# Optimization experiments

Measured on AMD Instinct MI355X. Metric: run time of the kernel, lower is better.

Reference implementation:

```python
import jax, jax.numpy as jnp
import numpy as np

# Per-chromosome bin counts: round(len/100000) for hg38 chromosome lengths (from __init__)
CHROM_BINS = [2490, 2422, 1983, 1902, 1815, 1708, 1593, 1451, 1384, 1338, 1351,
              1333, 1144, 1070, 1020, 903, 833, 804, 586, 644, 467, 508]
LOC = np.concatenate([[0], np.cumsum(CHROM_BINS)])  # 23 boundaries, LOC[-1] == 28749
TOTAL_BINS = int(LOC[-1])
COMP = 50          # compression_size
N_HEADS = 22
INPUT_DIM = N_HEADS * COMP * 2  # 2200
H1, H2, OUT = 1000, 50, 13
BATCH = 2048


def setup_inputs() -> dict:
    key = jax.random.key(0)
    ks = jax.random.split(key, 12)
    s = 0.02
    return {
        "input_tensor": jax.random.normal(ks[0], (BATCH, 2, TOTAL_BINS), jnp.float32),
        # all 22 head weight matrices concatenated along the input dim: (COMP, TOTAL_BINS)
        "head_w": jax.random.normal(ks[1], (COMP, TOTAL_BINS), jnp.float32) * s,
        "head_b": jax.random.normal(ks[2], (N_HEADS, COMP), jnp.float32) * s,
        "conc_w": jax.random.normal(ks[3], (INPUT_DIM, INPUT_DIM), jnp.float32) * s,
        "conc_b": jax.random.normal(ks[4], (INPUT_DIM,), jnp.float32) * s,
        "w1": jax.random.normal(ks[5], (H1, INPUT_DIM), jnp.float32) * s,
        "b1": jax.random.normal(ks[6], (H1,), jnp.float32) * s,
        "w2": jax.random.normal(ks[7], (H2, H1), jnp.float32) * s,
        "b2": jax.random.normal(ks[8], (H2,), jnp.float32) * s,
        "w3": jax.random.normal(ks[9], (OUT, H2), jnp.float32) * s,
        "b3": jax.random.normal(ks[10], (OUT,), jnp.float32) * s,
    }


def reference(input_tensor, head_w, head_b, conc_w, conc_b, w1, b1, w2, b2, w3, b3):
    # 22 per-chromosome heads, each applied to both channels; output order per
    # chromosome i is [head_i(ch0), head_i(ch1)], matching the torch loop.
    pieces = []
    for i in range(N_HEADS):
        a, b = int(LOC[i]), int(LOC[i + 1])
        seg = input_tensor[:, :, a:b]                       # (B, 2, L_i)
        h = jnp.einsum('bcl,ol->bco', seg, head_w[:, a:b]) + head_b[i]  # (B, 2, COMP)
        pieces.append(h.reshape(h.shape[0], -1))            # (B, 2*COMP)
    combined = jnp.concatenate(pieces, axis=1)              # (B, 2200)
    z = combined @ conc_w.T + conc_b                        # conc Linear
    # seq: Linear -> Dropout(eval=id) -> LeakyReLU -> Linear -> Dropout -> LeakyReLU -> Dropout -> Linear
    h1 = jax.nn.leaky_relu(z @ w1.T + b1, 0.01)
    h2 = jax.nn.leaky_relu(h1 @ w2.T + b2, 0.01)
    return h2 @ w3.T + b3                                   # (B, 13)
```

## Files before the change

kernel.cpp:

```cpp
#include <hip/hip_runtime.h>
#include <cstdint>

typedef __bf16 bf16_t;
typedef __bf16 bf16x4 __attribute__((ext_vector_type(4)));
typedef __bf16 bf16x8 __attribute__((ext_vector_type(8)));
typedef float  f32x4  __attribute__((ext_vector_type(4)));
typedef float  f32x4u __attribute__((ext_vector_type(4), aligned(4)));

#define TOTAL_BINS 28749
#define WH_LD64    29312
#define N_HEADS    22
#define BATCH      2048
#define ROWS       4096
#define IDIM       2200
#define IDIM_P     2208
#define IDIM_NP    2304
#define H1DIM      1000
#define H1_NP      1024
#define H2DIM      50
#define ODIM       13
#define KSPLIT     8

__constant__ int d_LOC[23]  = {0,2490,4912,6895,8797,10612,12320,13913,15364,16748,
                               18086,19437,20770,21914,22984,24004,24907,25740,26544,
                               27130,27774,28241,28749};
__constant__ int d_HA64[23] = {0,2496,4928,6912,8832,10688,12416,14016,15488,16896,
                               18240,19648,20992,22144,23232,24256,25216,26112,26944,
                               27584,28288,28800,29312};

__device__ __forceinline__ void g2lds16(const void* g, void* l) {
  __builtin_amdgcn_global_load_lds((const __attribute__((address_space(1))) void*)g,
                                   (__attribute__((address_space(3))) void*)l, 16, 0, 0);
}

__device__ __forceinline__ f32x4 mfma16(bf16x8 a, bf16x8 b, f32x4 c) {
  return __builtin_amdgcn_mfma_f32_16x16x32_bf16(a, b, c, 0, 0, 0);
}

__global__ __launch_bounds__(256) void convert_pad(const float* __restrict__ src,
                                                   bf16_t* __restrict__ dst,
                                                   int rows, int cols, int prow, int pcol)
{
  size_t i = (size_t)blockIdx.x * 256 + threadIdx.x;
  size_t total = (size_t)prow * pcol;
  if (i >= total) return;
  int r = (int)(i / pcol);
  int c = (int)(i - (size_t)r * pcol);
  float v = (r < rows && c < cols) ? src[(size_t)r * cols + c] : 0.0f;
  dst[i] = (bf16_t)v;
}

__global__ __launch_bounds__(256) void convert_headw(const float* __restrict__ src,
                                                     bf16_t* __restrict__ dst)
{
  size_t i = (size_t)blockIdx.x * 256 + threadIdx.x;
  if (i >= (size_t)64 * WH_LD64) return;
  int r = (int)(i / WH_LD64);
  int c = (int)(i - (size_t)r * WH_LD64);
  float v = 0.0f;
  #pragma unroll
  for (int h = 0; h < N_HEADS; h++) {
    int ha = d_HA64[h], hb = d_HA64[h + 1];
    if (c >= ha && c < hb) {
      int k = c - ha;
      int a = d_LOC[h];
      int L = d_LOC[h + 1] - a;
      if (r < 50 && k < L) v = src[(size_t)r * TOTAL_BINS + a + k];
    }
  }
  dst[i] = (bf16_t)v;
}

__global__ __launch_bounds__(256) void head_gemm2(const float* __restrict__ X,
                                                  const bf16_t* __restrict__ Wh,
                                                  const float* __restrict__ headb,
                                                  bf16_t* __restrict__ Cmb)
{
  __shared__ __attribute__((aligned(16))) bf16_t Ws[2][64][72];
  const int tid = threadIdx.x, lane = tid & 63, wid = tid >> 6;
  const int head = blockIdx.y;
  const int a   = d_LOC[head];
  const int ha  = d_HA64[head];
  const int L64 = d_HA64[head + 1] - ha;
  const int m0  = blockIdx.x * 64;
  const int la = lane & 15, lk = lane >> 4;
  const int wrow = m0 + wid * 16 + la;
  const uint32_t rowbase = (uint32_t)wrow * TOTAL_BINS + (uint32_t)a;
  const uint32_t MAX4 = (uint32_t)ROWS * TOTAL_BINS - 4;

  const int sn = tid >> 2, skg = (tid & 3) * 16;
  const bf16_t* wsrc = Wh + (size_t)sn * WH_LD64 + ha + skg;

  f32x4 acc[4] = {};

  #define LOADA(dst, kbase) do {                                     \
    uint32_t b0_ = (kbase) + (uint32_t)(lk * 8);                     \
    dst[0] = *(const f32x4u*)(X + min(b0_,      MAX4));              \
    dst[1] = *(const f32x4u*)(X + min(b0_ + 4,  MAX4));              \
    dst[2] = *(const f32x4u*)(X + min(b0_ + 32, MAX4));              \
    dst[3] = *(const f32x4u*)(X + min(b0_ + 36, MAX4));              \
  } while (0)

  {
    uint4 w0 = *(const uint4*)(wsrc);
    uint4 w1 = *(const uint4*)(wsrc + 8);
    *(uint4*)(&Ws[0][sn][skg])     = w0;
    *(uint4*)(&Ws[0][sn][skg + 8]) = w1;
  }
  f32x4u ar[4];
  LOADA(ar, rowbase);

  const int nIter = L64 >> 6;
  for (int i = 0; i < nIter; i++) {
    __syncthreads();
    const int cur = i & 1, nxt = cur ^ 1;
    uint4 nw0, nw1; f32x4u an[4];
    const bool more = (i + 1 < nIter);
    if (more) {
      const bf16_t* ws2 = wsrc + (size_t)(i + 1) * 64;
      nw0 = *(const uint4*)(ws2);
      nw1 = *(const uint4*)(ws2 + 8);
      LOADA(an, rowbase + (uint32_t)(i + 1) * 64);
    }
    bf16x8 af[2];
    #pragma unroll
    for (int kq = 0; kq < 2; kq++)
      #pragma unroll
      for (int j = 0; j < 8; j++)
        af[kq][j] = (bf16_t)ar[kq * 2 + (j >> 2)][j & 3];
    #pragma unroll
    for (int kq = 0; kq < 2; kq++)
      #pragma unroll
      for (int j = 0; j < 4; j++) {
        bf16x8 bf = *(const bf16x8*)(&Ws[cur][j * 16 + la][kq * 32 + lk * 8]);
        acc[j] = mfma16(af[kq], bf, acc[j]);
      }
    if (more) {
      *(uint4*)(&Ws[nxt][sn][skg])     = nw0;
      *(uint4*)(&Ws[nxt][sn][skg + 8]) = nw1;
      #pragma unroll
      for (int q = 0; q < 4; q++) ar[q] = an[q];
    }
  }

  #pragma unroll
  for (int j = 0; j < 4; j++) {
    int o = j * 16 + la;
    if (o < 50) {
      float bv = headb[head * 50 + o];
      #pragma unroll
      for (int r = 0; r < 4; r++) {
        int gr = m0 + wid * 16 + lk * 4 + r;
        Cmb[(size_t)(gr >> 1) * IDIM_P + head * 100 + (gr & 1) * 50 + o] =
            (bf16_t)(acc[j][r] + bv);
      }
    }
  }
  #undef LOADA
}

__global__ __launch_bounds__(256) void gemm_bt64(const bf16_t* __restrict__ A, int lda,
                                                 const bf16_t* __restrict__ W, int ldb,
                                                 const float* __restrict__ bias,
                                                 void* __restrict__ Cout, int ldc,
                                                 int K, int N, int act, int out_f32)
{
  __shared__ __attribute__((aligned(16))) bf16_t As[2][128][32];
  __shared__ __attribute__((aligned(16))) bf16_t Bs[2][64][32];
  const int tid  = threadIdx.x;
  const int lane = tid & 63, wid = tid >> 6;
  const int m0 = blockIdx.x * 128;
  const int n0 = blockIdx.y * 64;
  const int la = lane & 15, lk = lane >> 4;
  const int wm = wid * 32;

  f32x4 acc[2][4] = {};

  const bf16_t* asrc0 = A + (size_t)(m0 + (tid >> 2)) * lda + (tid & 3) * 8;
  const bf16_t* asrc1 = asrc0 + (size_t)64 * lda;
  const bf16_t* wsrc  = W + (size_t)(n0 + (tid >> 2)) * ldb + (tid & 3) * 8;

  auto stage = [&](int buf, int k0) {
    g2lds16(asrc0 + k0, &As[buf][0][0] + tid * 8);
    g2lds16(asrc1 + k0, &As[buf][64][0] + tid * 8);
    g2lds16(wsrc  + k0, &Bs[buf][0][0] + tid * 8);
  };
  stage(0, 0);

  int i = 0;
  for (int k0 = 0; k0 < K; k0 += 32, i++) {
    __syncthreads();
    const int cur = i & 1;
    if (k0 + 32 < K) stage(cur ^ 1, k0 + 32);
    bf16x8 af[2], bfr[4];
    #pragma unroll
    for (int ii = 0; ii < 2; ii++) af[ii]  = *(const bf16x8*)(&As[cur][wm + ii * 16 + la][lk * 8]);
    #pragma unroll
    for (int j = 0; j < 4; j++)    bfr[j] = *(const bf16x8*)(&Bs[cur][j * 16 + la][lk * 8]);
    #pragma unroll
    for (int ii = 0; ii < 2; ii++)
      #pragma unroll
      for (int j = 0; j < 4; j++)
        acc[ii][j] = mfma16(af[ii], bfr[j], acc[ii][j]);
  }

  float bv[4]; bool ok[4]; int gcv[4];
  #pragma unroll
  for (int j = 0; j < 4; j++) {
    int gc = n0 + j * 16 + la;
    gcv[j] = gc; ok[j] = gc < N;
    bv[j] = ok[j] ? bias[gc] : 0.0f;
  }
  #pragma unroll
  for (int ii = 0; ii < 2; ii++) {
    #pragma unroll
    for (int r = 0; r < 4; r++) {
      int gr = m0 + wm + ii * 16 + lk * 4 + r;
      #pragma unroll
      for (int j = 0; j < 4; j++) {
        if (ok[j]) {
          float v = acc[ii][j][r] + bv[j];
          if (act) v = fmaxf(v, 0.01f * v);
          if (out_f32) ((float*) Cout)[(size_t)gr * ldc + gcv[j]] = v;
          else         ((bf16_t*)Cout)[(size_t)gr * ldc + gcv[j]] = (bf16_t)v;
        }
      }
    }
  }
}

__global__ __launch_bounds__(256) void gemm_splitk(const bf16_t* __restrict__ A,
                                                   const bf16_t* __restrict__ W,
                                                   float* __restrict__ P)
{
  __shared__ __attribute__((aligned(16))) bf16_t As[2][128][32];
  __shared__ __attribute__((aligned(16))) bf16_t Bs[2][64][32];
  const int tid  = threadIdx.x;
  const int lane = tid & 63, wid = tid >> 6;
  const int m0 = blockIdx.x * 128;
  const int split = blockIdx.y;
  const int kb = split * (H1_NP / KSPLIT);
  const int la = lane & 15, lk = lane >> 4;
  const int wm = wid * 32;

  f32x4 acc[2][4] = {};

  const bf16_t* asrc0 = A + (size_t)(m0 + (tid >> 2)) * H1_NP + kb + (tid & 3) * 8;
  const bf16_t* asrc1 = asrc0 + (size_t)64 * H1_NP;
  const bf16_t* wsrc  = W + (size_t)(tid >> 2) * H1_NP + kb + (tid & 3) * 8;

  auto stage = [&](int buf, int k0) {
    g2lds16(asrc0 + k0, &As[buf][0][0] + tid * 8);
    g2lds16(asrc1 + k0, &As[buf][64][0] + tid * 8);
    g2lds16(wsrc  + k0, &Bs[buf][0][0] + tid * 8);
  };
  stage(0, 0);

  #pragma unroll
  for (int i = 0; i < 4; i++) {
    __syncthreads();
    const int cur = i & 1;
    if (i < 3) stage(cur ^ 1, (i + 1) * 32);
    bf16x8 af[2], bfr[4];
    #pragma unroll
    for (int ii = 0; ii < 2; ii++) af[ii]  = *(const bf16x8*)(&As[cur][wm + ii * 16 + la][lk * 8]);
    #pragma unroll
    for (int j = 0; j < 4; j++)    bfr[j] = *(const bf16x8*)(&Bs[cur][j * 16 + la][lk * 8]);
    #pragma unroll
    for (int ii = 0; ii < 2; ii++)
      #pragma unroll
      for (int j = 0; j < 4; j++)
        acc[ii][j] = mfma16(af[ii], bfr[j], acc[ii][j]);
  }

  #pragma unroll
  for (int ii = 0; ii < 2; ii++)
    #pragma unroll
    for (int r = 0; r < 4; r++) {
      int gr = m0 + wm + ii * 16 + lk * 4 + r;
      #pragma unroll
      for (int j = 0; j < 4; j++)
        P[((size_t)split * BATCH + gr) * 64 + j * 16 + la] = acc[ii][j][r];
    }
}

__global__ __launch_bounds__(256) void finalize_tail(const float* __restrict__ P,
                                                     const float* __restrict__ b2,
                                                     const float* __restrict__ w3,
                                                     const float* __restrict__ b3,
                                                     float* __restrict__ out)
{
  __shared__ float h2s[16][64];
  const int r0 = blockIdx.x * 16;
  const int t = threadIdx.x;
  const int r = t >> 4, c4 = (t & 15) * 4;
  f32x4 s = {};
  #pragma unroll
  for (int sp = 0; sp < KSPLIT; sp++) {
    const f32x4 v = *(const f32x4*)(P + ((size_t)sp * BATCH + r0 + r) * 64 + c4);
    s.x += v.x; s.y += v.y; s.z += v.z; s.w += v.w;
  }
  #pragma unroll
  for (int c = 0; c < 4; c++) {
    int col = c4 + c;
    float v = s[c] + ((col < H2DIM) ? b2[col] : 0.0f);
    h2s[r][col] = fmaxf(v, 0.01f * v);
  }
  __syncthreads();
  if (t < 16 * ODIM) {
    int rr = t / ODIM, o = t - rr * ODIM;
    float acc = b3[o];
    #pragma unroll 10
    for (int k = 0; k < H2DIM; k++) acc += h2s[rr][k] * w3[o * H2DIM + k];
    out[(size_t)(r0 + rr) * ODIM + o] = acc;
  }
}

extern "C" void kernel_launch(void* const* d_in, const int* in_sizes, int n_in,
                              void* d_out, int out_size, void* d_ws, size_t ws_size,
                              hipStream_t stream)
{
  const float* X      = (const float*)d_in[0];
  const float* head_w = (const float*)d_in[1];
  const float* head_b = (const float*)d_in[2];
  const float* conc_w = (const float*)d_in[3];
  const float* conc_b = (const float*)d_in[4];
  const float* w1     = (const float*)d_in[5];
  const float* b1     = (const float*)d_in[6];
  const float* w2     = (const float*)d_in[7];
  const float* b2     = (const float*)d_in[8];
  const float* w3     = (const float*)d_in[9];
  const float* b3     = (const float*)d_in[10];

  char* p = (char*)d_ws;
  auto alloc = [&](size_t bytes) { char* r = p; p += (bytes + 255) & ~(size_t)255; return r; };
  bf16_t* headw_ws = (bf16_t*)alloc((size_t)64 * WH_LD64 * 2);
  bf16_t* concw_ws = (bf16_t*)alloc((size_t)IDIM_NP * IDIM_P * 2);
  bf16_t* w1_ws    = (bf16_t*)alloc((size_t)H1_NP * IDIM_P * 2);
  bf16_t* w2_ws    = (bf16_t*)alloc((size_t)128 * H1_NP * 2);
  bf16_t* comb     = (bf16_t*)alloc((size_t)BATCH * IDIM_P * 2);
  bf16_t* zbuf     = (bf16_t*)alloc((size_t)BATCH * IDIM_P * 2);
  bf16_t* h1buf    = (bf16_t*)alloc((size_t)BATCH * H1_NP * 2);
  float*  h2p      = (float*) alloc((size_t)KSPLIT * BATCH * 64 * 4);

  auto cgrid = [](size_t n) { return dim3((unsigned)((n + 255) / 256)); };

  convert_headw<<<cgrid((size_t)64 * WH_LD64), 256, 0, stream>>>(head_w, headw_ws);
  convert_pad<<<cgrid((size_t)IDIM_NP * IDIM_P), 256, 0, stream>>>(conc_w, concw_ws, IDIM, IDIM, IDIM_NP, IDIM_P);
  convert_pad<<<cgrid((size_t)H1_NP * IDIM_P), 256, 0, stream>>>(w1, w1_ws, H1DIM, IDIM, H1_NP, IDIM_P);
  convert_pad<<<cgrid((size_t)128 * H1_NP), 256, 0, stream>>>(w2, w2_ws, H2DIM, H1DIM, 128, H1_NP);

  head_gemm2<<<dim3(ROWS / 64, N_HEADS), 256, 0, stream>>>(X, headw_ws, head_b, comb);

  gemm_bt64<<<dim3(BATCH / 128, IDIM_NP / 64), 256, 0, stream>>>(
      comb, IDIM_P, concw_ws, IDIM_P, conc_b, zbuf, IDIM_P, IDIM_P, IDIM, 0, 0);
  gemm_bt64<<<dim3(BATCH / 128, H1_NP / 64), 256, 0, stream>>>(
      zbuf, IDIM_P, w1_ws, IDIM_P, b1, h1buf, H1_NP, IDIM_P, H1DIM, 1, 0);

  gemm_splitk<<<dim3(BATCH / 128, KSPLIT), 256, 0, stream>>>(h1buf, w2_ws, h2p);
  finalize_tail<<<dim3(BATCH / 16), 256, 0, stream>>>(h2p, b2, w3, b3, (float*)d_out);
}
```

Baseline: 814.3 us.

## Vectorize weight conversion, swizzle GEMM LDS tiles, trim conc padding

The per-element weight conversion kernels are replaced with 8-wide versions that do two vector float4 loads and one 16-byte bf16 store per thread. The head-weight conversion now finds its head once instead of testing all 22 ranges per element. The GEMM kernels apply an XOR swizzle to the global source columns and the LDS read columns to cut LDS bank conflicts. The conc output padding drops from 2304 to 2240, which removes one tile column of blocks. Risks: the unaligned vector loads rely on 4-byte alignment, and the swizzle must match between load and read.

```diff
diff --git a/kernel.cpp b/kernel.cpp
--- a/kernel.cpp
+++ b/kernel.cpp
@@ -14,7 +14,7 @@
 #define ROWS       4096
 #define IDIM       2200
 #define IDIM_P     2208
-#define IDIM_NP    2304
+#define IDIM_NP    2240
 #define H1DIM      1000
 #define H1_NP      1024
 #define H2DIM      50
@@ -37,38 +37,60 @@
   return __builtin_amdgcn_mfma_f32_16x16x32_bf16(a, b, c, 0, 0, 0);
 }
 
-__global__ __launch_bounds__(256) void convert_pad(const float* __restrict__ src,
-                                                   bf16_t* __restrict__ dst,
-                                                   int rows, int cols, int prow, int pcol)
+__global__ __launch_bounds__(256) void convert_pad8(const float* __restrict__ src,
+                                                    bf16_t* __restrict__ dst,
+                                                    int rows, int cols, int prow, int pcol)
 {
   size_t i = (size_t)blockIdx.x * 256 + threadIdx.x;
-  size_t total = (size_t)prow * pcol;
-  if (i >= total) return;
-  int r = (int)(i / pcol);
-  int c = (int)(i - (size_t)r * pcol);
-  float v = (r < rows && c < cols) ? src[(size_t)r * cols + c] : 0.0f;
-  dst[i] = (bf16_t)v;
-}
-
-__global__ __launch_bounds__(256) void convert_headw(const float* __restrict__ src,
-                                                     bf16_t* __restrict__ dst)
+  int pc8 = pcol >> 3;
+  if (i >= (size_t)prow * pc8) return;
+  int r  = (int)(i / pc8);
+  int c0 = (int)(i - (size_t)r * pc8) * 8;
+  bf16x8 o;
+  if (r < rows && c0 + 8 <= cols) {
+    f32x4u a = *(const f32x4u*)(src + (size_t)r * cols + c0);
+    f32x4u b = *(const f32x4u*)(src + (size_t)r * cols + c0 + 4);
+    #pragma unroll
+    for (int j = 0; j < 4; j++) { o[j] = (bf16_t)a[j]; o[4 + j] = (bf16_t)b[j]; }
+  } else {
+    #pragma unroll
+    for (int j = 0; j < 8; j++) {
+      int c = c0 + j;
+      o[j] = (bf16_t)((r < rows && c < cols) ? src[(size_t)r * cols + c] : 0.0f);
+    }
+  }
+  *(bf16x8*)(dst + (size_t)r * pcol + c0) = o;
+}
+
+__global__ __launch_bounds__(256) void convert_headw8(const float* __restrict__ src,
+                                                      bf16_t* __restrict__ dst)
 {
   size_t i = (size_t)blockIdx.x * 256 + threadIdx.x;
-  if (i >= (size_t)64 * WH_LD64) return;
-  int r = (int)(i / WH_LD64);
-  int c = (int)(i - (size_t)r * WH_LD64);
-  float v = 0.0f;
-  #pragma unroll
-  for (int h = 0; h < N_HEADS; h++) {
-    int ha = d_HA64[h], hb = d_HA64[h + 1];
-    if (c >= ha && c < hb) {
-      int k = c - ha;
-      int a = d_LOC[h];
-      int L = d_LOC[h + 1] - a;
-      if (r < 50 && k < L) v = src[(size_t)r * TOTAL_BINS + a + k];
-    }
-  }
-  dst[i] = (bf16_t)v;
+  const int pc8 = WH_LD64 / 8;
+  if (i >= (size_t)64 * pc8) return;
+  int r  = (int)(i / pc8);
+  int c0 = (int)(i - (size_t)r * pc8) * 8;
+  int head = 0;
+  #pragma unroll
+  for (int h = 0; h < N_HEADS; h++) if (c0 >= d_HA64[h + 1]) head = h + 1;
+  const int ha = d_HA64[head], a = d_LOC[head];
+  const int L  = d_LOC[head + 1] - a;
+  const int k0 = c0 - ha;
+  bf16x8 o;
+  if (r < 50 && k0 + 8 <= L) {
+    const float* s = src + (size_t)r * TOTAL_BINS + a + k0;
+    f32x4u x = *(const f32x4u*)(s);
+    f32x4u y = *(const f32x4u*)(s + 4);
+    #pragma unroll
+    for (int j = 0; j < 4; j++) { o[j] = (bf16_t)x[j]; o[4 + j] = (bf16_t)y[j]; }
+  } else {
+    #pragma unroll
+    for (int j = 0; j < 8; j++) {
+      int k = k0 + j;
+      o[j] = (bf16_t)((r < 50 && k < L) ? src[(size_t)r * TOTAL_BINS + a + k] : 0.0f);
+    }
+  }
+  *(bf16x8*)(dst + (size_t)r * WH_LD64 + c0) = o;
 }
 
 __global__ __launch_bounds__(256) void head_gemm2(const float* __restrict__ X,
@@ -173,12 +195,14 @@
   const int n0 = blockIdx.y * 64;
   const int la = lane & 15, lk = lane >> 4;
   const int wm = wid * 32;
+  const int scg = (((tid & 3) ^ ((tid >> 3) & 3)) * 8);
+  const int lks = ((lk ^ ((la >> 1) & 3)) * 8);
 
   f32x4 acc[2][4] = {};
 
-  const bf16_t* asrc0 = A + (size_t)(m0 + (tid >> 2)) * lda + (tid & 3) * 8;
+  const bf16_t* asrc0 = A + (size_t)(m0 + (tid >> 2)) * lda + scg;
   const bf16_t* asrc1 = asrc0 + (size_t)64 * lda;
-  const bf16_t* wsrc  = W + (size_t)(n0 + (tid >> 2)) * ldb + (tid & 3) * 8;
+  const bf16_t* wsrc  = W + (size_t)(n0 + (tid >> 2)) * ldb + scg;
 
   auto stage = [&](int buf, int k0) {
     g2lds16(asrc0 + k0, &As[buf][0][0] + tid * 8);
@@ -194,9 +218,9 @@
     if (k0 + 32 < K) stage(cur ^ 1, k0 + 32);
     bf16x8 af[2], bfr[4];
     #pragma unroll
-    for (int ii = 0; ii < 2; ii++) af[ii]  = *(const bf16x8*)(&As[cur][wm + ii * 16 + la][lk * 8]);
-    #pragma unroll
-    for (int j = 0; j < 4; j++)    bfr[j] = *(const bf16x8*)(&Bs[cur][j * 16 + la][lk * 8]);
+    for (int ii = 0; ii < 2; ii++) af[ii]  = *(const bf16x8*)(&As[cur][wm + ii * 16 + la][lks]);
+    #pragma unroll
+    for (int j = 0; j < 4; j++)    bfr[j] = *(const bf16x8*)(&Bs[cur][j * 16 + la][lks]);
     #pragma unroll
     for (int ii = 0; ii < 2; ii++)
       #pragma unroll
@@ -242,12 +266,14 @@
   const int kb = split * (H1_NP / KSPLIT);
   const int la = lane & 15, lk = lane >> 4;
   const int wm = wid * 32;
+  const int scg = (((tid & 3) ^ ((tid >> 3) & 3)) * 8);
+  const int lks = ((lk ^ ((la >> 1) & 3)) * 8);
 
   f32x4 acc[2][4] = {};
 
-  const bf16_t* asrc0 = A + (size_t)(m0 + (tid >> 2)) * H1_NP + kb + (tid & 3) * 8;
+  const bf16_t* asrc0 = A + (size_t)(m0 + (tid >> 2)) * H1_NP + kb + scg;
   const bf16_t* asrc1 = asrc0 + (size_t)64 * H1_NP;
-  const bf16_t* wsrc  = W + (size_t)(tid >> 2) * H1_NP + kb + (tid & 3) * 8;
+  const bf16_t* wsrc  = W + (size_t)(tid >> 2) * H1_NP + kb + scg;
 
   auto stage = [&](int buf, int k0) {
     g2lds16(asrc0 + k0, &As[buf][0][0] + tid * 8);
@@ -263,9 +289,9 @@
     if (i < 3) stage(cur ^ 1, (i + 1) * 32);
     bf16x8 af[2], bfr[4];
     #pragma unroll
-    for (int ii = 0; ii < 2; ii++) af[ii]  = *(const bf16x8*)(&As[cur][wm + ii * 16 + la][lk * 8]);
-    #pragma unroll
-    for (int j = 0; j < 4; j++)    bfr[j] = *(const bf16x8*)(&Bs[cur][j * 16 + la][lk * 8]);
+    for (int ii = 0; ii < 2; ii++) af[ii]  = *(const bf16x8*)(&As[cur][wm + ii * 16 + la][lks]);
+    #pragma unroll
+    for (int j = 0; j < 4; j++)    bfr[j] = *(const bf16x8*)(&Bs[cur][j * 16 + la][lks]);
     #pragma unroll
     for (int ii = 0; ii < 2; ii++)
       #pragma unroll
@@ -345,10 +371,10 @@
 
   auto cgrid = [](size_t n) { return dim3((unsigned)((n + 255) / 256)); };
 
-  convert_headw<<<cgrid((size_t)64 * WH_LD64), 256, 0, stream>>>(head_w, headw_ws);
-  convert_pad<<<cgrid((size_t)IDIM_NP * IDIM_P), 256, 0, stream>>>(conc_w, concw_ws, IDIM, IDIM, IDIM_NP, IDIM_P);
-  convert_pad<<<cgrid((size_t)H1_NP * IDIM_P), 256, 0, stream>>>(w1, w1_ws, H1DIM, IDIM, H1_NP, IDIM_P);
-  convert_pad<<<cgrid((size_t)128 * H1_NP), 256, 0, stream>>>(w2, w2_ws, H2DIM, H1DIM, 128, H1_NP);
+  convert_headw8<<<cgrid((size_t)64 * WH_LD64 / 8), 256, 0, stream>>>(head_w, headw_ws);
+  convert_pad8<<<cgrid((size_t)IDIM_NP * IDIM_P / 8), 256, 0, stream>>>(conc_w, concw_ws, IDIM, IDIM, IDIM_NP, IDIM_P);
+  convert_pad8<<<cgrid((size_t)H1_NP * IDIM_P / 8), 256, 0, stream>>>(w1, w1_ws, H1DIM, IDIM, H1_NP, IDIM_P);
+  convert_pad8<<<cgrid((size_t)128 * H1_NP / 8), 256, 0, stream>>>(w2, w2_ws, H2DIM, H1DIM, 128, H1_NP);
 
   head_gemm2<<<dim3(ROWS / 64, N_HEADS), 256, 0, stream>>>(X, headw_ws, head_b, comb);
 
```

New measurement: 801.7 us. Within noise of the previous version (-1.6%).
